# Kernel optimization log

Hardware: AMD Instinct MI355X
Metric: run time of the kernel (lower is better)

Reference implementation:

```python
import jax, jax.numpy as jnp
import numpy as np

DIM = 768
HEADS = 12
HEAD_DIM = DIM // HEADS
B, N = 8, 512
LN_EPS = 1e-5


def setup_inputs() -> dict:
    key = jax.random.key(0)
    ks = jax.random.split(key, 6)
    x = jax.random.normal(ks[0], (B, N, DIM), dtype=jnp.float32)
    qkv_w = jax.random.normal(ks[1], (3 * DIM, DIM), dtype=jnp.float32) * (DIM ** -0.5)
    ln_w = jnp.ones((HEADS, N, N), dtype=jnp.float32)
    ln_b = jnp.zeros((HEADS, N, N), dtype=jnp.float32)
    proj_w = jax.random.normal(ks[2], (DIM, DIM), dtype=jnp.float32) * (DIM ** -0.5)
    proj_b = jnp.zeros((DIM,), dtype=jnp.float32)
    return {"x": x, "qkv_w": qkv_w, "ln_w": ln_w, "ln_b": ln_b,
            "proj_w": proj_w, "proj_b": proj_b}


def _grassmannian(t):
    # project each head vector onto the unit sphere (L2 normalize over head_dim)
    nrm = jnp.linalg.norm(t, axis=-1, keepdims=True)
    return t / nrm


def reference(x, qkv_w, ln_w, ln_b, proj_w, proj_b):
    b, n, c = x.shape
    qkv = (x @ qkv_w.T).reshape(b, n, 3, HEADS, HEAD_DIM)
    qkv = jnp.transpose(qkv, (2, 0, 3, 1, 4))  # (3, B, H, N, d)
    q, k, v = qkv[0], qkv[1], qkv[2]
    q = _grassmannian(q)
    k = _grassmannian(k)
    # ||outer(q_n, k_m)||_2^2 over head_dim == sum_d q_d^2 k_d^2 = (q^2) @ (k^2)^T
    attn = jnp.einsum('bhnd,bhmd->bhnm', q * q, k * k)  # (B, H, N, N)
    # LayerNorm over normalized_shape=(H, N, N), i.e. per batch element
    mean = jnp.mean(attn, axis=(1, 2, 3), keepdims=True)
    var = jnp.var(attn, axis=(1, 2, 3), keepdims=True)
    attn = (attn - mean) * jax.lax.rsqrt(var + LN_EPS) * ln_w + ln_b
    out = jnp.einsum('bhnm,bhmd->bhnd', attn, v)  # (B, H, N, d)
    out = jnp.transpose(out, (0, 2, 1, 3)).reshape(b, n, c)
    out = out @ proj_w.T + proj_b
    return out, attn
```

## Files before the change

kernel.cpp:

```cpp
#include <hip/hip_runtime.h>

typedef __attribute__((ext_vector_type(8))) short bf16x8;
typedef __attribute__((ext_vector_type(4))) float f32x4;

#define HEADS 12
#define NN 512
#define BB 8
#define DIM 768
#define LDK 72
#define OUT0_ELEMS ((size_t)BB*NN*DIM)

__device__ __forceinline__ ushort f2bf(float f) {
  union { float f; uint u; } v; v.f = f;
  uint r = v.u + 0x7fffu + ((v.u >> 16) & 1u);
  return (ushort)(r >> 16);
}

__global__ __launch_bounds__(256) void cvt3_kernel(
    const float* __restrict__ a, ushort* __restrict__ oa, int na8,
    const float* __restrict__ b, ushort* __restrict__ ob, int nb8,
    const float* __restrict__ c, ushort* __restrict__ oc, int nc8) {
  int i = blockIdx.x * 256 + threadIdx.x;
  const float* in; ushort* out;
  if (i < na8) { in = a; out = oa; }
  else if (i < na8 + nb8) { i -= na8; in = b; out = ob; }
  else { i -= na8 + nb8; if (i >= nc8) return; in = c; out = oc; }
  float4 x = ((const float4*)in)[i*2], y = ((const float4*)in)[i*2+1];
  uint4 o;
  o.x = f2bf(x.x) | ((uint)f2bf(x.y) << 16);
  o.y = f2bf(x.z) | ((uint)f2bf(x.w) << 16);
  o.z = f2bf(y.x) | ((uint)f2bf(y.y) << 16);
  o.w = f2bf(y.z) | ((uint)f2bf(y.w) << 16);
  ((uint4*)out)[i] = o;
}

__global__ __launch_bounds__(256) void qkv_gemm(
    const ushort* __restrict__ xb, const ushort* __restrict__ wb,
    ushort* __restrict__ q2b, ushort* __restrict__ k2b, ushort* __restrict__ vt)
{
  __shared__ ushort As[128 * LDK];
  __shared__ ushort Bs[128 * LDK];
  const int t = threadIdx.x, l = t & 63, w = t >> 6;
  const int bx = blockIdx.x, by = blockIdx.y;
  const int rowbase = by * 128, colbase = bx * 128;
  const int wr = w >> 1, wc = w & 1, lr = l & 15, lg = l >> 4;
  f32x4 acc[4][4] = {};

  for (int kc = 0; kc < DIM; kc += 64) {
    #pragma unroll
    for (int i = 0; i < 4; ++i) {
      int c = t + 256 * i;
      int r = c >> 3, k16 = c & 7;
      *(uint4*)(As + r * LDK + k16 * 8) =
          *(const uint4*)(xb + (size_t)(rowbase + r) * DIM + kc + k16 * 8);
      *(uint4*)(Bs + r * LDK + k16 * 8) =
          *(const uint4*)(wb + (size_t)(colbase + r) * DIM + kc + k16 * 8);
    }
    __syncthreads();
    #pragma unroll
    for (int ks = 0; ks < 2; ++ks) {
      bf16x8 af[4], bg[4];
      #pragma unroll
      for (int i = 0; i < 4; ++i)
        af[i] = *(const bf16x8*)(As + (wr*64 + i*16 + lr) * LDK + ks*32 + lg*8);
      #pragma unroll
      for (int j = 0; j < 4; ++j)
        bg[j] = *(const bf16x8*)(Bs + (wc*64 + j*16 + lr) * LDK + ks*32 + lg*8);
      #pragma unroll
      for (int i = 0; i < 4; ++i)
        #pragma unroll
        for (int j = 0; j < 4; ++j)
          acc[i][j] = __builtin_amdgcn_mfma_f32_16x16x32_bf16(af[i], bg[j], acc[i][j], 0, 0, 0);
    }
    __syncthreads();
  }

  const int gcol = colbase + wc * 64;
  const int sel = gcol / DIM;
  const int h = (gcol % DIM) / 64;
  if (sel < 2) {
    ushort* dst = (sel == 0) ? q2b : k2b;
    #pragma unroll
    for (int i = 0; i < 4; ++i) {
      #pragma unroll
      for (int r = 0; r < 4; ++r) {
        float vj[4]; float s = 0.f;
        #pragma unroll
        for (int j = 0; j < 4; ++j) { vj[j] = acc[i][j][r]; s += vj[j] * vj[j]; }
        #pragma unroll
        for (int off = 1; off < 16; off <<= 1) s += __shfl_xor(s, off);
        float inv = 1.0f / s;
        int row = rowbase + wr*64 + i*16 + lg*4 + r;
        int b = row >> 9, n = row & 511;
        ushort* o = dst + (((size_t)(b * HEADS + h) * NN + n) << 6);
        #pragma unroll
        for (int j = 0; j < 4; ++j) o[j*16 + lr] = f2bf(vj[j] * vj[j] * inv);
      }
    }
  } else {
    #pragma unroll
    for (int i = 0; i < 4; ++i) {
      int row0 = rowbase + wr*64 + i*16 + lg*4;
      int b = row0 >> 9, n0 = row0 & 511;
      #pragma unroll
      for (int j = 0; j < 4; ++j) {
        int d = j*16 + lr;
        ushort4 pk;
        pk.x = f2bf(acc[i][j][0]); pk.y = f2bf(acc[i][j][1]);
        pk.z = f2bf(acc[i][j][2]); pk.w = f2bf(acc[i][j][3]);
        *(ushort4*)(vt + (((size_t)(b * HEADS + h) * 64 + d) << 9) + n0) = pk;
      }
    }
  }
}

__global__ __launch_bounds__(256) void stats_kernel(
    const ushort* __restrict__ q2b, const ushort* __restrict__ k2b,
    double* __restrict__ hsum)
{
  __shared__ ushort Ks[128 * LDK];
  __shared__ float red[8];
  const int t = threadIdx.x, l = t & 63, w = t >> 6;
  const int rt = blockIdx.x, h = blockIdx.y, b = blockIdx.z;
  const size_t bh = (size_t)(b * HEADS + h);
  const int rowbase = rt * 64;
  const int lr = l & 15, lg = l >> 4;
  bf16x8 af[2];
  #pragma unroll
  for (int ks = 0; ks < 2; ++ks)
    af[ks] = *(const bf16x8*)(q2b + (bh << 15) +
                              ((size_t)(rowbase + w*16 + lr) << 6) + ks*32 + lg*8);
  float s1 = 0.f, s2 = 0.f;
  for (int ct = 0; ct < 4; ++ct) {
    #pragma unroll
    for (int i = 0; i < 4; ++i) {
      int c = t + 256 * i;
      int r = c >> 3, k16 = c & 7;
      *(uint4*)(Ks + r * LDK + k16 * 8) =
          *(const uint4*)(k2b + (bh << 15) + ((size_t)(ct*128 + r) << 6) + k16 * 8);
    }
    __syncthreads();
    #pragma unroll
    for (int j = 0; j < 8; ++j) {
      bf16x8 b0 = *(const bf16x8*)(Ks + (j*16 + lr) * LDK + lg*8);
      bf16x8 b1 = *(const bf16x8*)(Ks + (j*16 + lr) * LDK + 32 + lg*8);
      f32x4 a = {};
      a = __builtin_amdgcn_mfma_f32_16x16x32_bf16(af[0], b0, a, 0, 0, 0);
      a = __builtin_amdgcn_mfma_f32_16x16x32_bf16(af[1], b1, a, 0, 0, 0);
      #pragma unroll
      for (int r = 0; r < 4; ++r) { s1 += a[r]; s2 += a[r]*a[r]; }
    }
    __syncthreads();
  }
  #pragma unroll
  for (int off = 1; off < 64; off <<= 1) { s1 += __shfl_xor(s1, off); s2 += __shfl_xor(s2, off); }
  if (l == 0) { red[w] = s1; red[4 + w] = s2; }
  __syncthreads();
  if (t == 0) {
    double d1 = (double)red[0] + red[1] + red[2] + red[3];
    double d2 = (double)red[4] + red[5] + red[6] + red[7];
    atomicAdd(&hsum[b * 2], d1);
    atomicAdd(&hsum[b * 2 + 1], d2);
  }
}

__global__ __launch_bounds__(256) void norm_pv(
    const ushort* __restrict__ q2b, const ushort* __restrict__ k2b,
    const ushort* __restrict__ vt,
    const float* __restrict__ lnw, const float* __restrict__ lnb,
    const double* __restrict__ hsum,
    float* __restrict__ attn, ushort* __restrict__ obh)
{
  __shared__ ushort Pb[64 * 128];
  const int t = threadIdx.x, l = t & 63, w = t >> 6;
  const int rt = blockIdx.x, h = blockIdx.y, b = blockIdx.z;
  const size_t bh = (size_t)(b * HEADS + h);
  const int rowbase = rt * 64;
  const int lr = l & 15, lg = l >> 4;
  const double cnt = (double)HEADS * NN * NN;
  double mu = hsum[b * 2] / cnt;
  double var = hsum[b * 2 + 1] / cnt - mu * mu;
  const float mean = (float)mu;
  const float istd = (float)(1.0 / sqrt(var + 1e-5));

  bf16x8 qf[4][2];
  #pragma unroll
  for (int j = 0; j < 4; ++j)
    #pragma unroll
    for (int ks = 0; ks < 2; ++ks)
      qf[j][ks] = *(const bf16x8*)(q2b + (bh << 15) +
                    ((size_t)(rowbase + j*16 + lr) << 6) + ks*32 + lg*8);

  f32x4 opv[4] = {};

  for (int ct = 0; ct < 4; ++ct) {
    #pragma unroll
    for (int i = 0; i < 2; ++i) {
      const ushort* krow = k2b + (bh << 15) +
                           ((size_t)(ct*128 + w*32 + i*16 + lr) << 6);
      bf16x8 a0 = *(const bf16x8*)(krow + lg*8);
      bf16x8 a1 = *(const bf16x8*)(krow + 32 + lg*8);
      const int mloc = w*32 + i*16 + lg*4;
      const int m0 = ct*128 + mloc;
      const int cch = mloc >> 3;
      #pragma unroll
      for (int j = 0; j < 4; ++j) {
        f32x4 a = {};
        a = __builtin_amdgcn_mfma_f32_16x16x32_bf16(a0, qf[j][0], a, 0, 0, 0);
        a = __builtin_amdgcn_mfma_f32_16x16x32_bf16(a1, qf[j][1], a, 0, 0, 0);
        const int n = j*16 + lr;
        const size_t rowoff = ((size_t)h * NN + rowbase + n) * NN + m0;
        const float4 lw4 = *(const float4*)(lnw + rowoff);
        const float4 lb4 = *(const float4*)(lnb + rowoff);
        f32x4 v;
        v[0] = (a[0] - mean) * istd * lw4.x + lb4.x;
        v[1] = (a[1] - mean) * istd * lw4.y + lb4.y;
        v[2] = (a[2] - mean) * istd * lw4.z + lb4.z;
        v[3] = (a[3] - mean) * istd * lw4.w + lb4.w;
        __builtin_nontemporal_store(v,
            (f32x4*)(attn + ((bh << 9) + rowbase + n) * NN + m0));
        uint pk01, pk23;
        asm("v_cvt_pk_bf16_f32 %0, %1, %2" : "=v"(pk01) : "v"(v[0]), "v"(v[1]));
        asm("v_cvt_pk_bf16_f32 %0, %1, %2" : "=v"(pk23) : "v"(v[2]), "v"(v[3]));
        const int pch = (cch & 8) | ((cch & 7) ^ (n & 7));
        uint2 pk = { pk01, pk23 };
        *(uint2*)(Pb + n*128 + pch*8 + (lg & 1)*4) = pk;
      }
    }
    __syncthreads();
    #pragma unroll
    for (int ks = 0; ks < 4; ++ks) {
      const int cc = ks*4 + lg;
      const int nl = w*16 + lr;
      const int pch = (cc & 8) | ((cc & 7) ^ (nl & 7));
      bf16x8 ap = *(const bf16x8*)(Pb + nl*128 + pch*8);
      #pragma unroll
      for (int j = 0; j < 4; ++j) {
        bf16x8 bv = *(const bf16x8*)(vt + (bh << 15) +
                      ((size_t)(j*16 + lr) << 9) + ct*128 + ks*32 + lg*8);
        opv[j] = __builtin_amdgcn_mfma_f32_16x16x32_bf16(ap, bv, opv[j], 0, 0, 0);
      }
    }
    __syncthreads();
  }
  #pragma unroll
  for (int j = 0; j < 4; ++j) {
    int gc = h * 64 + j*16 + lr;
    #pragma unroll
    for (int r = 0; r < 4; ++r) {
      int gr = b * NN + rowbase + w*16 + lg*4 + r;
      obh[(size_t)gr * DIM + gc] = f2bf(opv[j][r]);
    }
  }
}

__global__ __launch_bounds__(256) void proj_gemm(
    const ushort* __restrict__ obh, const ushort* __restrict__ pwb,
    const float* __restrict__ pb, float* __restrict__ out)
{
  __shared__ ushort As[128 * LDK];
  __shared__ ushort Bs[128 * LDK];
  const int t = threadIdx.x, l = t & 63, w = t >> 6;
  const int bx = blockIdx.x, by = blockIdx.y;
  const int rowbase = by * 128, colbase = bx * 128;
  const int wr = w >> 1, wc = w & 1, lr = l & 15, lg = l >> 4;
  f32x4 acc[4][4] = {};
  for (int kc = 0; kc < DIM; kc += 64) {
    #pragma unroll
    for (int i = 0; i < 4; ++i) {
      int c = t + 256 * i;
      int r = c >> 3, k16 = c & 7;
      *(uint4*)(As + r * LDK + k16 * 8) =
          *(const uint4*)(obh + (size_t)(rowbase + r) * DIM + kc + k16 * 8);
      *(uint4*)(Bs + r * LDK + k16 * 8) =
          *(const uint4*)(pwb + (size_t)(colbase + r) * DIM + kc + k16 * 8);
    }
    __syncthreads();
    #pragma unroll
    for (int ks = 0; ks < 2; ++ks) {
      bf16x8 af[4], bg[4];
      #pragma unroll
      for (int i = 0; i < 4; ++i)
        af[i] = *(const bf16x8*)(As + (wr*64 + i*16 + lr) * LDK + ks*32 + lg*8);
      #pragma unroll
      for (int j = 0; j < 4; ++j)
        bg[j] = *(const bf16x8*)(Bs + (wc*64 + j*16 + lr) * LDK + ks*32 + lg*8);
      #pragma unroll
      for (int i = 0; i < 4; ++i)
        #pragma unroll
        for (int j = 0; j < 4; ++j)
          acc[i][j] = __builtin_amdgcn_mfma_f32_16x16x32_bf16(af[i], bg[j], acc[i][j], 0, 0, 0);
    }
    __syncthreads();
  }
  #pragma unroll
  for (int i = 0; i < 4; ++i) {
    #pragma unroll
    for (int r = 0; r < 4; ++r) {
      int row = rowbase + wr*64 + i*16 + lg*4 + r;
      #pragma unroll
      for (int j = 0; j < 4; ++j) {
        int col = colbase + wc*64 + j*16 + lr;
        out[(size_t)row * DIM + col] = acc[i][j][r] + pb[col];
      }
    }
  }
}

extern "C" void kernel_launch(void* const* d_in, const int* in_sizes, int n_in,
                              void* d_out, int out_size, void* d_ws, size_t ws_size,
                              hipStream_t stream) {
  const float* x      = (const float*)d_in[0];
  const float* qkv_w  = (const float*)d_in[1];
  const float* ln_w   = (const float*)d_in[2];
  const float* ln_b   = (const float*)d_in[3];
  const float* proj_w = (const float*)d_in[4];
  const float* proj_b = (const float*)d_in[5];
  float* out      = (float*)d_out;
  float* attn_out = out + OUT0_ELEMS;

  char* ws = (char*)d_ws;
  double* hsum = (double*)ws;
  ushort* wb   = (ushort*)(ws + 256);
  ushort* pwb  = wb  + (size_t)2304 * 768;
  ushort* xb   = pwb + (size_t)768 * 768;
  ushort* q2b  = xb  + (size_t)4096 * 768;
  ushort* k2b  = q2b + ((size_t)BB * HEADS * NN << 6);
  ushort* vt   = k2b + ((size_t)BB * HEADS * NN << 6);
  ushort* obh  = vt  + ((size_t)BB * HEADS * NN << 6);

  hipMemsetAsync(hsum, 0, 128, stream);
  cvt3_kernel<<<dim3(2688), 256, 0, stream>>>(qkv_w, wb, 221184,
                                              proj_w, pwb, 73728,
                                              x, xb, 393216);
  qkv_gemm    <<<dim3(18, 32),        256, 0, stream>>>(xb, wb, q2b, k2b, vt);
  stats_kernel<<<dim3(8, HEADS, BB),  256, 0, stream>>>(q2b, k2b, hsum);
  norm_pv     <<<dim3(8, HEADS, BB),  256, 0, stream>>>(q2b, k2b, vt, ln_w, ln_b, hsum,
                                                        attn_out, obh);
  proj_gemm   <<<dim3(6, 32),         256, 0, stream>>>(obh, pwb, proj_b, out);
}
```

Baseline: 293.9 us.

## Split attention write into separate LN kernel with LDS-staged coalesced stores

Splits the fused normalize+PV kernel in two. A new ln_write kernel recomputes QK^T and applies the layer norm, then stages each 32-row tile in swizzled shared memory so the attention map is written to global memory with fully contiguous row stores. pv_kernel recomputes the same scores only to feed the PV product, without writing attn. The intent is better coalescing of the large fp32 attention write. The cost is computing QK^T and reading ln_w/ln_b twice, plus an extra kernel launch.

```diff
diff --git a/kernel.cpp b/kernel.cpp
--- a/kernel.cpp
+++ b/kernel.cpp
@@ -164,12 +164,73 @@
   }
 }
 
-__global__ __launch_bounds__(256) void norm_pv(
+__global__ __launch_bounds__(256) void ln_write(
+    const ushort* __restrict__ q2b, const ushort* __restrict__ k2b,
+    const float* __restrict__ lnw, const float* __restrict__ lnb,
+    const double* __restrict__ hsum, float* __restrict__ attn)
+{
+  __shared__ float Sl[32 * 512];
+  const int t = threadIdx.x, l = t & 63, w = t >> 6;
+  const int rt = blockIdx.x, h = blockIdx.y, b = blockIdx.z;
+  const size_t bh = (size_t)(b * HEADS + h);
+  const int rowbase = rt * 32;
+  const int lr = l & 15, lg = l >> 4;
+  const double cnt = (double)HEADS * NN * NN;
+  double mu = hsum[b * 2] / cnt;
+  double var = hsum[b * 2 + 1] / cnt - mu * mu;
+  const float mean = (float)mu;
+  const float istd = (float)(1.0 / sqrt(var + 1e-5));
+
+  bf16x8 qf[2][2];
+  #pragma unroll
+  for (int j = 0; j < 2; ++j)
+    #pragma unroll
+    for (int ks = 0; ks < 2; ++ks)
+      qf[j][ks] = *(const bf16x8*)(q2b + (bh << 15) +
+                    ((size_t)(rowbase + j*16 + lr) << 6) + ks*32 + lg*8);
+
+  #pragma unroll
+  for (int i = 0; i < 8; ++i) {
+    const ushort* krow = k2b + (bh << 15) + ((size_t)(w*128 + i*16 + lr) << 6);
+    bf16x8 a0 = *(const bf16x8*)(krow + lg*8);
+    bf16x8 a1 = *(const bf16x8*)(krow + 32 + lg*8);
+    const int m0 = w*128 + i*16 + lg*4;
+    const int cbase = m0 >> 2;
+    #pragma unroll
+    for (int j = 0; j < 2; ++j) {
+      f32x4 a = {};
+      a = __builtin_amdgcn_mfma_f32_16x16x32_bf16(a0, qf[j][0], a, 0, 0, 0);
+      a = __builtin_amdgcn_mfma_f32_16x16x32_bf16(a1, qf[j][1], a, 0, 0, 0);
+      const int n = j*16 + lr;
+      const size_t rowoff = ((size_t)h * NN + rowbase + n) * NN + m0;
+      const float4 lw4 = *(const float4*)(lnw + rowoff);
+      const float4 lb4 = *(const float4*)(lnb + rowoff);
+      f32x4 v;
+      v[0] = (a[0] - mean) * istd * lw4.x + lb4.x;
+      v[1] = (a[1] - mean) * istd * lw4.y + lb4.y;
+      v[2] = (a[2] - mean) * istd * lw4.z + lb4.z;
+      v[3] = (a[3] - mean) * istd * lw4.w + lb4.w;
+      const int cs = cbase ^ (n & 7);
+      *(f32x4*)((char*)Sl + n*2048 + cs*16) = v;
+    }
+  }
+  __syncthreads();
+  float* dst = attn + ((bh << 9) + rowbase) * NN;
+  #pragma unroll
+  for (int it = 0; it < 16; ++it) {
+    const int f = it*1024 + t*4;
+    const int n = f >> 9, c2 = (f >> 2) & 127;
+    const int cs = c2 ^ (n & 7);
+    f32x4 v = *(const f32x4*)((const char*)Sl + n*2048 + cs*16);
+    __builtin_nontemporal_store(v, (f32x4*)(dst + f));
+  }
+}
+
+__global__ __launch_bounds__(256) void pv_kernel(
     const ushort* __restrict__ q2b, const ushort* __restrict__ k2b,
     const ushort* __restrict__ vt,
     const float* __restrict__ lnw, const float* __restrict__ lnb,
-    const double* __restrict__ hsum,
-    float* __restrict__ attn, ushort* __restrict__ obh)
+    const double* __restrict__ hsum, ushort* __restrict__ obh)
 {
   __shared__ ushort Pb[64 * 128];
   const int t = threadIdx.x, l = t & 63, w = t >> 6;
@@ -217,8 +278,6 @@
         v[1] = (a[1] - mean) * istd * lw4.y + lb4.y;
         v[2] = (a[2] - mean) * istd * lw4.z + lb4.z;
         v[3] = (a[3] - mean) * istd * lw4.w + lb4.w;
-        __builtin_nontemporal_store(v,
-            (f32x4*)(attn + ((bh << 9) + rowbase + n) * NN + m0));
         uint pk01, pk23;
         asm("v_cvt_pk_bf16_f32 %0, %1, %2" : "=v"(pk01) : "v"(v[0]), "v"(v[1]));
         asm("v_cvt_pk_bf16_f32 %0, %1, %2" : "=v"(pk23) : "v"(v[2]), "v"(v[3]));
@@ -335,7 +394,7 @@
                                               x, xb, 393216);
   qkv_gemm    <<<dim3(18, 32),        256, 0, stream>>>(xb, wb, q2b, k2b, vt);
   stats_kernel<<<dim3(8, HEADS, BB),  256, 0, stream>>>(q2b, k2b, hsum);
-  norm_pv     <<<dim3(8, HEADS, BB),  256, 0, stream>>>(q2b, k2b, vt, ln_w, ln_b, hsum,
-                                                        attn_out, obh);
+  ln_write    <<<dim3(16, HEADS, BB), 256, 0, stream>>>(q2b, k2b, ln_w, ln_b, hsum, attn_out);
+  pv_kernel   <<<dim3(8, HEADS, BB),  256, 0, stream>>>(q2b, k2b, vt, ln_w, ln_b, hsum, obh);
   proj_gemm   <<<dim3(6, 32),         256, 0, stream>>>(obh, pwb, proj_b, out);
 }
```

Result: slower. 318.1 us (+8.2%).
